# Kernel optimization log

Measured on AMD Instinct MI355X. Metric: run time of the kernel, lower is better.

## Reference

```python
import jax, jax.numpy as jnp
import numpy as np

EMBED_DIM = 1024
NUM_HEADS = 16
HEAD_DIM = EMBED_DIM // NUM_HEADS


def setup_inputs() -> dict:
    key = jax.random.key(0)
    ks = jax.random.split(key, 5)
    B, N, D = 4, 2048, EMBED_DIM
    scale = 1.0 / np.sqrt(D)
    return {
        "x": jax.random.normal(ks[0], (B, N, D), dtype=jnp.float32),
        "w_qkv": jax.random.normal(ks[1], (D, 3 * D), dtype=jnp.float32) * scale,
        "b_qkv": jnp.zeros((3 * D,), dtype=jnp.float32),
        "w_proj": jax.random.normal(ks[2], (D, D), dtype=jnp.float32) * scale,
        "b_proj": jnp.zeros((D,), dtype=jnp.float32),
    }


def reference(x, w_qkv, b_qkv, w_proj, b_proj):
    B, N, D = x.shape
    H, Hd = NUM_HEADS, HEAD_DIM
    qkv = x @ w_qkv + b_qkv                      # [B, N, 3D]
    # 'b n (three h d) -> three b h n d'
    qkv = qkv.reshape(B, N, 3, H, Hd).transpose(2, 0, 3, 1, 4)
    q, k, v = qkv[0], qkv[1], qkv[2]             # each [B, H, N, Hd]
    scores = jnp.einsum('bhnd,bhmd->bhnm', q, k) / np.sqrt(Hd)
    probs = jax.nn.softmax(scores, axis=-1)      # dropout is identity in eval
    out = jnp.einsum('bhnm,bhmd->bhnd', probs, v)
    out = out.transpose(0, 2, 1, 3).reshape(B, N, D)  # 'b h n d -> b n (h d)'
    return out @ w_proj + b_proj
```

## Files before the change

### kernel.cpp

```cpp
#include <hip/hip_runtime.h>
#include <hip/hip_bf16.h>

#define DEVI __device__ __forceinline__

typedef float f32x4  __attribute__((ext_vector_type(4)));
typedef float f32x16 __attribute__((ext_vector_type(16)));
typedef short bf16x8 __attribute__((ext_vector_type(8)));
typedef int   i32x4  __attribute__((ext_vector_type(4)));

constexpr int BATCH = 4;
constexpr int SEQ   = 2048;
constexpr int DIM   = 1024;
constexpr int NH    = 16;
constexpr int HD    = 64;
constexpr int TD    = 3 * DIM;
constexpr int MTOT  = BATCH * SEQ;

constexpr float QSCALE = 0.125f * 1.44269504f;

DEVI unsigned short f2bf(float f) {
    __hip_bfloat16 h = __float2bfloat16(f);
    return *reinterpret_cast<unsigned short*>(&h);
}

DEVI void gload_lds16(const unsigned short* gsrc, unsigned short* ldst) {
    __builtin_amdgcn_global_load_lds(
        (const __attribute__((address_space(1))) void*)gsrc,
        (__attribute__((address_space(3))) void*)ldst,
        16, 0, 0);
}

__global__ void cvt_kernel(const float* __restrict__ in, unsigned short* __restrict__ out, int n4) {
    int i = blockIdx.x * blockDim.x + threadIdx.x;
    int stride = gridDim.x * blockDim.x;
    for (; i < n4; i += stride) {
        float4 v = reinterpret_cast<const float4*>(in)[i];
        ushort4 o;
        o.x = f2bf(v.x); o.y = f2bf(v.y); o.z = f2bf(v.z); o.w = f2bf(v.w);
        reinterpret_cast<ushort4*>(out)[i] = o;
    }
}

__global__ void transp_kernel(const float* __restrict__ in, unsigned short* __restrict__ out, int R, int C) {
    __shared__ float tile[32][33];
    int c0 = blockIdx.x * 32, r0 = blockIdx.y * 32;
    int tx = threadIdx.x, ty = threadIdx.y;
#pragma unroll
    for (int i = 0; i < 32; i += 8)
        tile[ty + i][tx] = in[(long)(r0 + ty + i) * C + c0 + tx];
    __syncthreads();
#pragma unroll
    for (int i = 0; i < 32; i += 8)
        out[(long)(c0 + ty + i) * R + r0 + tx] = f2bf(tile[tx][ty + i]);
}

template <bool OUT_BF16>
__global__ __launch_bounds__(256) void gemm_bt_kernel(
    const unsigned short* __restrict__ A,
    const unsigned short* __restrict__ Bt,
    const float* __restrict__ bias,
    void* __restrict__ Cout,
    int M, int Nn, int K, int scale_ncols, float scl)
{
    __shared__ unsigned short As[128 * 32];
    __shared__ unsigned short Bs[128 * 32];

    const int t  = threadIdx.x;
    const int l  = t & 63;
    const int w  = t >> 6;
    const int wr = w >> 1, wc = w & 1;
    const int lrow = l & 15, lk = l >> 4;

    const int gx  = gridDim.x;
    const int nwg = gx * gridDim.y;
    const int orig = blockIdx.y * gx + blockIdx.x;
    const int xcd = orig & 7, idx = orig >> 3;
    const int q8 = nwg >> 3, r8 = nwg & 7;
    const int swz = (xcd < r8 ? xcd * (q8 + 1) : r8 * (q8 + 1) + (xcd - r8) * q8) + idx;
    const int tr = swz / gx, tc = swz - tr * gx;

    f32x4 acc[4][4] = {};

    const int r0  = t >> 2;
    const int ch0 = t & 3;
    const long arow_base = (long)(tr * 128) * K;
    const long brow_base = (long)(tc * 128) * K;

    const int nk = K >> 5;
    for (int kt = 0; kt < nk; ++kt) {
        const int kb = kt * 32;
        gload_lds16(A  + arow_base + (long)r0 * K        + kb + ch0 * 8, &As[t * 8]);
        gload_lds16(A  + arow_base + (long)(r0 + 64) * K + kb + ch0 * 8, &As[(t + 256) * 8]);
        gload_lds16(Bt + brow_base + (long)r0 * K        + kb + ch0 * 8, &Bs[t * 8]);
        gload_lds16(Bt + brow_base + (long)(r0 + 64) * K + kb + ch0 * 8, &Bs[(t + 256) * 8]);
        __syncthreads();

        bf16x8 a[4], bb[4];
#pragma unroll
        for (int mi = 0; mi < 4; ++mi)
            a[mi] = *(const bf16x8*)&As[(wr * 64 + mi * 16 + lrow) * 32 + lk * 8];
#pragma unroll
        for (int ni = 0; ni < 4; ++ni)
            bb[ni] = *(const bf16x8*)&Bs[(wc * 64 + ni * 16 + lrow) * 32 + lk * 8];
#pragma unroll
        for (int mi = 0; mi < 4; ++mi)
#pragma unroll
            for (int ni = 0; ni < 4; ++ni)
                acc[mi][ni] = __builtin_amdgcn_mfma_f32_16x16x32_bf16(a[mi], bb[ni], acc[mi][ni], 0, 0, 0);
        __syncthreads();
    }

    const int row_base = tr * 128 + wr * 64;
    const int col_base = tc * 128 + wc * 64;
    const float mult = (col_base < scale_ncols) ? scl : 1.0f;
    float bv[4];
#pragma unroll
    for (int ni = 0; ni < 4; ++ni) bv[ni] = bias[col_base + ni * 16 + lrow];

#pragma unroll
    for (int mi = 0; mi < 4; ++mi)
#pragma unroll
        for (int ni = 0; ni < 4; ++ni)
#pragma unroll
            for (int r = 0; r < 4; ++r) {
                int row = row_base + mi * 16 + lk * 4 + r;
                int col = col_base + ni * 16 + lrow;
                float v = (acc[mi][ni][r] + bv[ni]) * mult;
                if (OUT_BF16) ((unsigned short*)Cout)[(long)row * Nn + col] = f2bf(v);
                else          ((float*)Cout)[(long)row * Nn + col] = v;
            }
}

__global__ __launch_bounds__(256, 2) void attn_kernel(
    const unsigned short* __restrict__ qkv,
    unsigned short* __restrict__ aout)
{
    constexpr int KVB  = 128;
    constexpr int PADW = 72;
    constexpr int VROW = 136;
    __shared__ unsigned short Ks[KVB * PADW];
    __shared__ unsigned short VsT[HD * VROW];

    const int t = threadIdx.x;
    const int l = t & 63;
    const int ln = l & 31;
    const int hi = l >> 5;

    const int b  = blockIdx.y >> 4;
    const int h  = blockIdx.y & 15;
    const int q0 = blockIdx.x * 128 + (t >> 6) * 32;

    bf16x8 bq[4];
    {
        const long qrow = (long)(b * SEQ + q0 + ln) * TD + h * HD;
#pragma unroll
        for (int s = 0; s < 4; ++s)
            bq[s] = *(const bf16x8*)&qkv[qrow + s * 16 + hi * 8];
    }

    f32x16 o[2];
#pragma unroll
    for (int i = 0; i < 16; ++i) { o[0][i] = 0.f; o[1][i] = 0.f; }
    float lsum = 0.f;

    const long kbase = (long)(b * SEQ) * TD + DIM + h * HD;
    const long vbase = (long)(b * SEQ) * TD + 2 * DIM + h * HD;

    const int krow = t & 63, kc0 = (t >> 6) * 8;
    const int vch = t >> 5, vrp = t & 31;

    i32x4 kr0, kr1, kr2, kr3, vr0, vr1, vr2, vr3;

#define LOAD_TILE(m0) do {                                                     \
        const unsigned short* kp = &qkv[kbase + (long)((m0) + krow) * TD + kc0]; \
        kr0 = *(const i32x4*)kp;                                               \
        kr1 = *(const i32x4*)(kp + 32);                                        \
        kr2 = *(const i32x4*)(kp + 64 * TD);                                   \
        kr3 = *(const i32x4*)(kp + 64 * TD + 32);                              \
        const unsigned short* vp = &qkv[vbase + (long)((m0) + 4 * vrp) * TD + vch * 8]; \
        vr0 = *(const i32x4*)vp;                                               \
        vr1 = *(const i32x4*)(vp + TD);                                        \
        vr2 = *(const i32x4*)(vp + 2 * TD);                                    \
        vr3 = *(const i32x4*)(vp + 3 * TD);                                    \
    } while (0)

#define WRITE_TILE() do {                                                      \
        *(i32x4*)&Ks[krow * PADW + kc0]             = kr0;                     \
        *(i32x4*)&Ks[krow * PADW + kc0 + 32]        = kr1;                     \
        *(i32x4*)&Ks[(64 + krow) * PADW + kc0]      = kr2;                     \
        *(i32x4*)&Ks[(64 + krow) * PADW + kc0 + 32] = kr3;                     \
        const unsigned short* u0 = (const unsigned short*)&vr0;                \
        const unsigned short* u1 = (const unsigned short*)&vr1;                \
        const unsigned short* u2 = (const unsigned short*)&vr2;                \
        const unsigned short* u3 = (const unsigned short*)&vr3;                \
        unsigned int* V32 = (unsigned int*)VsT;           \
        _Pragma("unroll")                                                      \
        for (int j = 0; j < 8; ++j) {                                          \
            unsigned int wa = (unsigned int)u0[j] | ((unsigned int)u1[j] << 16); \
            unsigned int wb = (unsigned int)u2[j] | ((unsigned int)u3[j] << 16); \
            V32[(vch * 8 + j) * 68 + 2 * vrp]     = wa;                        \
            V32[(vch * 8 + j) * 68 + 2 * vrp + 1] = wb;                        \
        }                                                                      \
    } while (0)

#define SUB(koff) do {                                                         \
        f32x16 sv[2];                                                          \
        __builtin_amdgcn_s_setprio(1);                                         \
        _Pragma("unroll")                                                      \
        for (int f = 0; f < 2; ++f) {                                          \
            f32x16 acc = {};                                                   \
            _Pragma("unroll")                                                  \
            for (int s = 0; s < 4; ++s) {                                      \
                bf16x8 ak = *(const bf16x8*)&Ks[((koff) + f * 32 + ln) * PADW + s * 16 + hi * 8]; \
                acc = __builtin_amdgcn_mfma_f32_32x32x16_bf16(ak, bq[s], acc, 0, 0, 0); \
            }                                                                  \
            sv[f] = acc;                                                       \
        }                                                                      \
        __builtin_amdgcn_s_setprio(0);                                         \
        _Pragma("unroll")                                                      \
        for (int f = 0; f < 2; ++f)                                            \
            _Pragma("unroll")                                                  \
            for (int i = 0; i < 16; ++i)                                       \
                sv[f][i] = exp2f(sv[f][i]);                                    \
        {                                                                      \
            float s8[8];                                                       \
            _Pragma("unroll")                                                  \
            for (int i = 0; i < 8; ++i)                                        \
                s8[i] = (sv[0][i] + sv[0][i + 8]) + (sv[1][i] + sv[1][i + 8]); \
            float s4a = s8[0] + s8[1], s4b = s8[2] + s8[3];                    \
            float s4c = s8[4] + s8[5], s4d = s8[6] + s8[7];                    \
            lsum += (s4a + s4b) + (s4c + s4d);                                 \
        }                                                                      \
        bf16x8 pb[4];                                                          \
        _Pragma("unroll")                                                      \
        for (int ks = 0; ks < 4; ++ks) {                                       \
            const int f = ks >> 1, base = (ks & 1) * 8;                        \
            unsigned x0, x1, y0, y1;                                           \
            asm("v_cvt_pk_bf16_f32 %0, %1, %2" : "=v"(x0) : "v"(sv[f][base + 0]), "v"(sv[f][base + 1])); \
            asm("v_cvt_pk_bf16_f32 %0, %1, %2" : "=v"(x1) : "v"(sv[f][base + 2]), "v"(sv[f][base + 3])); \
            asm("v_cvt_pk_bf16_f32 %0, %1, %2" : "=v"(y0) : "v"(sv[f][base + 4]), "v"(sv[f][base + 5])); \
            asm("v_cvt_pk_bf16_f32 %0, %1, %2" : "=v"(y1) : "v"(sv[f][base + 6]), "v"(sv[f][base + 7])); \
            asm("v_permlane32_swap_b32 %0, %1" : "+v"(x0), "+v"(y0));          \
            asm("v_permlane32_swap_b32 %0, %1" : "+v"(x1), "+v"(y1));          \
            union { unsigned u[4]; bf16x8 v; } pu;                             \
            pu.u[0] = x0; pu.u[1] = x1; pu.u[2] = y0; pu.u[3] = y1;            \
            pb[ks] = pu.v;                                                     \
        }                                                                      \
        __builtin_amdgcn_s_setprio(1);                                         \
        _Pragma("unroll")                                                      \
        for (int f2 = 0; f2 < 2; ++f2)                                         \
            _Pragma("unroll")                                                  \
            for (int ks = 0; ks < 4; ++ks) {                                   \
                bf16x8 av = *(const bf16x8*)&VsT[(f2 * 32 + ln) * VROW + (koff) + ks * 16 + hi * 8]; \
                o[f2] = __builtin_amdgcn_mfma_f32_32x32x16_bf16(av, pb[ks], o[f2], 0, 0, 0); \
            }                                                                  \
        __builtin_amdgcn_s_setprio(0);                                         \
    } while (0)

    LOAD_TILE(0);
    WRITE_TILE();
    __syncthreads();

    for (int m0 = 0; m0 < SEQ; m0 += KVB) {
        const int mn = (m0 + KVB) & (SEQ - 1);
        LOAD_TILE(mn);

        SUB(0);
        SUB(64);

        __syncthreads();
        WRITE_TILE();
        __syncthreads();
    }

#undef LOAD_TILE
#undef WRITE_TILE
#undef SUB

    lsum += __shfl_xor(lsum, 32);

    float inv = 1.0f / lsum;
    const long orow = (long)(b * SEQ + q0 + ln);
#pragma unroll
    for (int f2 = 0; f2 < 2; ++f2)
#pragma unroll
        for (int g = 0; g < 4; ++g) {
            ushort4 st;
            st.x = f2bf(o[f2][4 * g + 0] * inv);
            st.y = f2bf(o[f2][4 * g + 1] * inv);
            st.z = f2bf(o[f2][4 * g + 2] * inv);
            st.w = f2bf(o[f2][4 * g + 3] * inv);
            *(ushort4*)&aout[orow * DIM + h * HD + f2 * 32 + 8 * g + 4 * hi] = st;
        }
}

extern "C" void kernel_launch(void* const* d_in, const int* in_sizes, int n_in,
                              void* d_out, int out_size, void* d_ws, size_t ws_size,
                              hipStream_t stream)
{
    const float* x      = (const float*)d_in[0];
    const float* w_qkv  = (const float*)d_in[1];
    const float* b_qkv  = (const float*)d_in[2];
    const float* w_proj = (const float*)d_in[3];
    const float* b_proj = (const float*)d_in[4];
    float* out = (float*)d_out;

    unsigned short* x_bf   = (unsigned short*)d_ws;
    unsigned short* wqkvT  = x_bf   + (size_t)MTOT * DIM;
    unsigned short* wprojT = wqkvT  + (size_t)TD * DIM;
    unsigned short* qkv    = wprojT + (size_t)DIM * DIM;
    unsigned short* attn   = qkv    + (size_t)MTOT * TD;

    cvt_kernel<<<2048, 256, 0, stream>>>(x, x_bf, MTOT * DIM / 4);
    dim3 tb(32, 8);
    transp_kernel<<<dim3(TD / 32, DIM / 32), tb, 0, stream>>>(w_qkv, wqkvT, DIM, TD);
    transp_kernel<<<dim3(DIM / 32, DIM / 32), tb, 0, stream>>>(w_proj, wprojT, DIM, DIM);

    gemm_bt_kernel<true><<<dim3(TD / 128, MTOT / 128), 256, 0, stream>>>(
        x_bf, wqkvT, b_qkv, qkv, MTOT, TD, DIM, DIM, QSCALE);

    attn_kernel<<<dim3(SEQ / 128, BATCH * NH), 256, 0, stream>>>(qkv, attn);

    gemm_bt_kernel<false><<<dim3(DIM / 128, MTOT / 128), 256, 0, stream>>>(
        attn, wprojT, b_proj, out, MTOT, DIM, DIM, 0, 1.0f);
}
```

Before: 238.4 us.

## Software-pipeline attention loop: overlap QK^T of next tile with PV of previous

Restructures the attention inner loop to use 64-row KV tiles in double-buffered LDS (K and V ping-pong). Each iteration computes QK^T for the current tile, then PV for the previous tile's probabilities, then exp/pack, so the MFMA work of the two matmuls is interleaved with the softmax VALU work. It adds a prologue and epilogue and more LDS buffers, and syncs twice per 64-row tile instead of twice per 128-row tile.

```diff
diff --git a/kernel.cpp b/kernel.cpp
--- a/kernel.cpp
+++ b/kernel.cpp
@@ -135,11 +135,10 @@
     const unsigned short* __restrict__ qkv,
     unsigned short* __restrict__ aout)
 {
-    constexpr int KVB  = 128;
+    constexpr int KVB  = 64;
     constexpr int PADW = 72;
-    constexpr int VROW = 136;
-    __shared__ unsigned short Ks[KVB * PADW];
-    __shared__ unsigned short VsT[HD * VROW];
+    __shared__ unsigned short Ks0[KVB * PADW], Ks1[KVB * PADW];
+    __shared__ unsigned short Vs0[HD * PADW],  Vs1[HD * PADW];
 
     const int t = threadIdx.x;
     const int l = t & 63;
@@ -162,6 +161,7 @@
 #pragma unroll
     for (int i = 0; i < 16; ++i) { o[0][i] = 0.f; o[1][i] = 0.f; }
     float lsum = 0.f;
+    bf16x8 pb[4];
 
     const long kbase = (long)(b * SEQ) * TD + DIM + h * HD;
     const long vbase = (long)(b * SEQ) * TD + 2 * DIM + h * HD;
@@ -169,113 +169,130 @@
     const int krow = t & 63, kc0 = (t >> 6) * 8;
     const int vch = t >> 5, vrp = t & 31;
 
-    i32x4 kr0, kr1, kr2, kr3, vr0, vr1, vr2, vr3;
-
-#define LOAD_TILE(m0) do {                                                     \
+    i32x4 kr0, kr1, vr0, vr1;
+
+#define LOAD_T(m0) do {                                                        \
         const unsigned short* kp = &qkv[kbase + (long)((m0) + krow) * TD + kc0]; \
         kr0 = *(const i32x4*)kp;                                               \
         kr1 = *(const i32x4*)(kp + 32);                                        \
-        kr2 = *(const i32x4*)(kp + 64 * TD);                                   \
-        kr3 = *(const i32x4*)(kp + 64 * TD + 32);                              \
-        const unsigned short* vp = &qkv[vbase + (long)((m0) + 4 * vrp) * TD + vch * 8]; \
+        const unsigned short* vp = &qkv[vbase + (long)((m0) + 2 * vrp) * TD + vch * 8]; \
         vr0 = *(const i32x4*)vp;                                               \
         vr1 = *(const i32x4*)(vp + TD);                                        \
-        vr2 = *(const i32x4*)(vp + 2 * TD);                                    \
-        vr3 = *(const i32x4*)(vp + 3 * TD);                                    \
-    } while (0)
-
-#define WRITE_TILE() do {                                                      \
-        *(i32x4*)&Ks[krow * PADW + kc0]             = kr0;                     \
-        *(i32x4*)&Ks[krow * PADW + kc0 + 32]        = kr1;                     \
-        *(i32x4*)&Ks[(64 + krow) * PADW + kc0]      = kr2;                     \
-        *(i32x4*)&Ks[(64 + krow) * PADW + kc0 + 32] = kr3;                     \
+    } while (0)
+
+#define WRITE_T(KD, VD) do {                                                   \
+        *(i32x4*)&(KD)[krow * PADW + kc0]      = kr0;                          \
+        *(i32x4*)&(KD)[krow * PADW + kc0 + 32] = kr1;                          \
         const unsigned short* u0 = (const unsigned short*)&vr0;                \
         const unsigned short* u1 = (const unsigned short*)&vr1;                \
-        const unsigned short* u2 = (const unsigned short*)&vr2;                \
-        const unsigned short* u3 = (const unsigned short*)&vr3;                \
-        unsigned int* V32 = (unsigned int*)VsT;           \
+        unsigned int* V32 = (unsigned int*)(VD);                               \
         _Pragma("unroll")                                                      \
         for (int j = 0; j < 8; ++j) {                                          \
-            unsigned int wa = (unsigned int)u0[j] | ((unsigned int)u1[j] << 16); \
-            unsigned int wb = (unsigned int)u2[j] | ((unsigned int)u3[j] << 16); \
-            V32[(vch * 8 + j) * 68 + 2 * vrp]     = wa;                        \
-            V32[(vch * 8 + j) * 68 + 2 * vrp + 1] = wb;                        \
+            unsigned int word = (unsigned int)u0[j] | ((unsigned int)u1[j] << 16); \
+            V32[(vch * 8 + j) * 36 + vrp] = word;                              \
         }                                                                      \
     } while (0)
 
-#define SUB(koff) do {                                                         \
-        f32x16 sv[2];                                                          \
+#define QKT(KC, sv) do {                                                       \
         __builtin_amdgcn_s_setprio(1);                                         \
         _Pragma("unroll")                                                      \
         for (int f = 0; f < 2; ++f) {                                          \
             f32x16 acc = {};                                                   \
             _Pragma("unroll")                                                  \
             for (int s = 0; s < 4; ++s) {                                      \
-                bf16x8 ak = *(const bf16x8*)&Ks[((koff) + f * 32 + ln) * PADW + s * 16 + hi * 8]; \
+                bf16x8 ak = *(const bf16x8*)&(KC)[(f * 32 + ln) * PADW + s * 16 + hi * 8]; \
                 acc = __builtin_amdgcn_mfma_f32_32x32x16_bf16(ak, bq[s], acc, 0, 0, 0); \
             }                                                                  \
-            sv[f] = acc;                                                       \
+            (sv)[f] = acc;                                                     \
         }                                                                      \
         __builtin_amdgcn_s_setprio(0);                                         \
+    } while (0)
+
+#define PVOP(VD) do {                                                          \
+        __builtin_amdgcn_s_setprio(1);                                         \
+        _Pragma("unroll")                                                      \
+        for (int f2 = 0; f2 < 2; ++f2)                                         \
+            _Pragma("unroll")                                                  \
+            for (int ks = 0; ks < 4; ++ks) {                                   \
+                bf16x8 av = *(const bf16x8*)&(VD)[(f2 * 32 + ln) * PADW + ks * 16 + hi * 8]; \
+                o[f2] = __builtin_amdgcn_mfma_f32_32x32x16_bf16(av, pb[ks], o[f2], 0, 0, 0); \
+            }                                                                  \
+        __builtin_amdgcn_s_setprio(0);                                         \
+    } while (0)
+
+#define SMPACK(sv) do {                                                        \
         _Pragma("unroll")                                                      \
         for (int f = 0; f < 2; ++f)                                            \
             _Pragma("unroll")                                                  \
             for (int i = 0; i < 16; ++i)                                       \
-                sv[f][i] = exp2f(sv[f][i]);                                    \
+                (sv)[f][i] = exp2f((sv)[f][i]);                                \
         {                                                                      \
             float s8[8];                                                       \
             _Pragma("unroll")                                                  \
             for (int i = 0; i < 8; ++i)                                        \
-                s8[i] = (sv[0][i] + sv[0][i + 8]) + (sv[1][i] + sv[1][i + 8]); \
+                s8[i] = ((sv)[0][i] + (sv)[0][i + 8]) + ((sv)[1][i] + (sv)[1][i + 8]); \
             float s4a = s8[0] + s8[1], s4b = s8[2] + s8[3];                    \
             float s4c = s8[4] + s8[5], s4d = s8[6] + s8[7];                    \
             lsum += (s4a + s4b) + (s4c + s4d);                                 \
         }                                                                      \
-        bf16x8 pb[4];                                                          \
         _Pragma("unroll")                                                      \
         for (int ks = 0; ks < 4; ++ks) {                                       \
             const int f = ks >> 1, base = (ks & 1) * 8;                        \
             unsigned x0, x1, y0, y1;                                           \
-            asm("v_cvt_pk_bf16_f32 %0, %1, %2" : "=v"(x0) : "v"(sv[f][base + 0]), "v"(sv[f][base + 1])); \
-            asm("v_cvt_pk_bf16_f32 %0, %1, %2" : "=v"(x1) : "v"(sv[f][base + 2]), "v"(sv[f][base + 3])); \
-            asm("v_cvt_pk_bf16_f32 %0, %1, %2" : "=v"(y0) : "v"(sv[f][base + 4]), "v"(sv[f][base + 5])); \
-            asm("v_cvt_pk_bf16_f32 %0, %1, %2" : "=v"(y1) : "v"(sv[f][base + 6]), "v"(sv[f][base + 7])); \
+            asm("v_cvt_pk_bf16_f32 %0, %1, %2" : "=v"(x0) : "v"((sv)[f][base + 0]), "v"((sv)[f][base + 1])); \
+            asm("v_cvt_pk_bf16_f32 %0, %1, %2" : "=v"(x1) : "v"((sv)[f][base + 2]), "v"((sv)[f][base + 3])); \
+            asm("v_cvt_pk_bf16_f32 %0, %1, %2" : "=v"(y0) : "v"((sv)[f][base + 4]), "v"((sv)[f][base + 5])); \
+            asm("v_cvt_pk_bf16_f32 %0, %1, %2" : "=v"(y1) : "v"((sv)[f][base + 6]), "v"((sv)[f][base + 7])); \
             asm("v_permlane32_swap_b32 %0, %1" : "+v"(x0), "+v"(y0));          \
             asm("v_permlane32_swap_b32 %0, %1" : "+v"(x1), "+v"(y1));          \
             union { unsigned u[4]; bf16x8 v; } pu;                             \
             pu.u[0] = x0; pu.u[1] = x1; pu.u[2] = y0; pu.u[3] = y1;            \
             pb[ks] = pu.v;                                                     \
         }                                                                      \
-        __builtin_amdgcn_s_setprio(1);                                         \
-        _Pragma("unroll")                                                      \
-        for (int f2 = 0; f2 < 2; ++f2)                                         \
-            _Pragma("unroll")                                                  \
-            for (int ks = 0; ks < 4; ++ks) {                                   \
-                bf16x8 av = *(const bf16x8*)&VsT[(f2 * 32 + ln) * VROW + (koff) + ks * 16 + hi * 8]; \
-                o[f2] = __builtin_amdgcn_mfma_f32_32x32x16_bf16(av, pb[ks], o[f2], 0, 0, 0); \
-            }                                                                  \
-        __builtin_amdgcn_s_setprio(0);                                         \
-    } while (0)
-
-    LOAD_TILE(0);
-    WRITE_TILE();
+    } while (0)
+
+#define ITER(next_off, KC, VPREV, KW, VW) do {                                 \
+        LOAD_T(next_off);                                                      \
+        f32x16 sv[2];                                                          \
+        QKT(KC, sv);                                                           \
+        PVOP(VPREV);                                                           \
+        SMPACK(sv);                                                            \
+        __syncthreads();                                                       \
+        WRITE_T(KW, VW);                                                       \
+        __syncthreads();                                                       \
+    } while (0)
+
+    LOAD_T(0);
+    WRITE_T(Ks0, Vs0);
     __syncthreads();
-
-    for (int m0 = 0; m0 < SEQ; m0 += KVB) {
-        const int mn = (m0 + KVB) & (SEQ - 1);
-        LOAD_TILE(mn);
-
-        SUB(0);
-        SUB(64);
-
-        __syncthreads();
-        WRITE_TILE();
-        __syncthreads();
-    }
-
-#undef LOAD_TILE
-#undef WRITE_TILE
-#undef SUB
+    LOAD_T(KVB);
+    {
+        f32x16 sv[2];
+        QKT(Ks0, sv);
+        SMPACK(sv);
+    }
+    WRITE_T(Ks1, Vs1);
+    __syncthreads();
+
+    for (int m = 0; m < 15; ++m) {
+        ITER((2 * m + 2) * KVB, Ks1, Vs0, Ks0, Vs0);
+        ITER((2 * m + 3) * KVB, Ks0, Vs1, Ks1, Vs1);
+    }
+
+    {
+        f32x16 sv[2];
+        QKT(Ks1, sv);
+        PVOP(Vs0);
+        SMPACK(sv);
+    }
+    PVOP(Vs1);
+
+#undef LOAD_T
+#undef WRITE_T
+#undef QKT
+#undef PVOP
+#undef SMPACK
+#undef ITER
 
     lsum += __shfl_xor(lsum, 32);
 
```

Result: faster. 227.3 us (-4.7%).
